# Performance work log

Hardware: AMD Instinct MI355X
Metric: run time of the kernel (lower is better)

The kernel has to match this reference:

```python
import jax, jax.numpy as jnp
import numpy as np

V, E, HID, T = 50000, 256, 512, 12   # vocab, embed dim, lstm hidden (bi total), tagset size
START, STOP = 10, 11
L = 2048                              # sentence length
H = HID // 2                          # per-direction hidden
NEG = -10000.0


def setup_inputs():
    key = jax.random.key(0)
    ks = jax.random.split(key, 13)
    s = 0.05
    sentence = jax.random.randint(ks[0], (L,), 0, V)
    embed = jax.random.normal(ks[1], (V, E), jnp.float32) * s
    w_ih_f = jax.random.normal(ks[2], (4 * H, E), jnp.float32) * s
    w_hh_f = jax.random.normal(ks[3], (4 * H, H), jnp.float32) * s
    b_ih_f = jax.random.normal(ks[4], (4 * H,), jnp.float32) * s
    b_hh_f = jax.random.normal(ks[5], (4 * H,), jnp.float32) * s
    w_ih_b = jax.random.normal(ks[6], (4 * H, E), jnp.float32) * s
    w_hh_b = jax.random.normal(ks[7], (4 * H, H), jnp.float32) * s
    b_ih_b = jax.random.normal(ks[8], (4 * H,), jnp.float32) * s
    b_hh_b = jax.random.normal(ks[9], (4 * H,), jnp.float32) * s
    w_out = jax.random.normal(ks[10], (T, HID), jnp.float32) * s
    b_out = jax.random.normal(ks[11], (T,), jnp.float32) * s
    transitions = jax.random.normal(ks[12], (T, T), jnp.float32)
    transitions = transitions.at[START, :].set(NEG).at[:, STOP].set(NEG)
    return dict(sentence=sentence, embed=embed,
                w_ih_f=w_ih_f, w_hh_f=w_hh_f, b_ih_f=b_ih_f, b_hh_f=b_hh_f,
                w_ih_b=w_ih_b, w_hh_b=w_hh_b, b_ih_b=b_ih_b, b_hh_b=b_hh_b,
                w_out=w_out, b_out=b_out, transitions=transitions)


def _lstm_dir(x, w_ih, w_hh, b, reverse):
    # x: [L, E] -> hs: [L, H]; PyTorch gate order i, f, g, o
    xg = x @ w_ih.T + b  # [L, 4H] precomputed input contribution

    def step(carry, xg_t):
        h, c = carry
        g = xg_t + h @ w_hh.T
        i, f, gg, o = jnp.split(g, 4)
        i, f, o = jax.nn.sigmoid(i), jax.nn.sigmoid(f), jax.nn.sigmoid(o)
        c = f * c + i * jnp.tanh(gg)
        h = o * jnp.tanh(c)
        return (h, c), h

    hdim = w_hh.shape[1]
    init = (jnp.zeros((hdim,), x.dtype), jnp.zeros((hdim,), x.dtype))
    _, hs = jax.lax.scan(step, init, xg, reverse=reverse)
    return hs


def _lstm_feats(sentence, embed, w_ih_f, w_hh_f, b_ih_f, b_hh_f,
                w_ih_b, w_hh_b, b_ih_b, b_hh_b, w_out, b_out):
    x = embed[sentence]                                        # [L, E]
    hf = _lstm_dir(x, w_ih_f, w_hh_f, b_ih_f + b_hh_f, False)  # [L, H]
    hb = _lstm_dir(x, w_ih_b, w_hh_b, b_ih_b + b_hh_b, True)   # [L, H]
    h = jnp.concatenate([hf, hb], axis=-1)                     # [L, 2H]
    return h @ w_out.T + b_out                                 # [L, T]


def reference(sentence, embed, w_ih_f, w_hh_f, b_ih_f, b_hh_f,
              w_ih_b, w_hh_b, b_ih_b, b_hh_b, w_out, b_out, transitions):
    feats = _lstm_feats(sentence, embed, w_ih_f, w_hh_f, b_ih_f, b_hh_f,
                        w_ih_b, w_hh_b, b_ih_b, b_hh_b, w_out, b_out)

    # Viterbi DP vectorized over tags, scanned over time
    init_v = jnp.full((T,), NEG, feats.dtype).at[START].set(0.0)

    def vstep(v, feat):
        scores = transitions + v[None, :]        # [next_tag, prev_tag]
        bp = jnp.argmax(scores, axis=1)          # best previous tag per next tag
        v_new = jnp.max(scores, axis=1) + feat
        return v_new, bp

    v, bps = jax.lax.scan(vstep, init_v, feats)  # bps: [L, T]
    terminal = v + transitions[STOP]
    best = jnp.argmax(terminal)
    path_score = terminal[best]

    def btrack(tag, bp):
        return bp[tag], tag

    _, best_path = jax.lax.scan(btrack, best, bps, reverse=True)  # [L] tags
    return path_score, best_path
```

## Files before the change

### kernel.cpp

```cpp
#include <hip/hip_runtime.h>

#define LSEQ 2048
#define TAGS 12

typedef _Float16 half2v __attribute__((ext_vector_type(2)));
typedef unsigned long long u64;

__device__ __forceinline__ float sigm(float x){ return 1.0f/(1.0f+__expf(-x)); }
__device__ __forceinline__ float tanh_fast(float x){ return 1.0f - 2.0f/(1.0f+__expf(2.0f*x)); }
__device__ __forceinline__ half2v pack2(float a, float b){
  half2v r; r.x=(_Float16)a; r.y=(_Float16)b; return r;
}

__global__ void init_kernel(u64* ex)
{
  int tid = blockIdx.x*256 + threadIdx.x;
  if (tid < 1024) ex[tid] = 0ull;
}

__global__ void xg_kernel(
    const int* sent, const float* embed,
    const float* w_ih_f, const float* b_ih_f, const float* b_hh_f,
    const float* w_ih_b, const float* b_ih_b, const float* b_hh_b,
    float* xg)
{
  __shared__ float x_sh[8][256];
  int tid = threadIdx.x;
  int t0 = blockIdx.x * 8;
  for (int i=0;i<8;++i){
    int idx = sent[t0+i];
    x_sh[i][tid] = embed[(size_t)idx*256 + tid];
  }
  __syncthreads();
  for (int ri=0; ri<8; ++ri){
    int r = ri*256 + tid;
    int d = r >> 10;
    int row = r & 1023;
    const float* wr = (d ? w_ih_b : w_ih_f) + (size_t)row*256;
    const float* bi = d ? b_ih_b : b_ih_f;
    const float* bh = d ? b_hh_b : b_hh_f;
    float acc[8];
    #pragma unroll
    for (int i=0;i<8;++i) acc[i]=0.f;
    for (int k0=0;k0<256;k0+=4){
      float4 p = *(const float4*)(wr + k0);
      #pragma unroll
      for (int i=0;i<8;++i){
        acc[i] += p.x*x_sh[i][k0] + p.y*x_sh[i][k0+1]
                + p.z*x_sh[i][k0+2] + p.w*x_sh[i][k0+3];
      }
    }
    float bias = bi[row] + bh[row];
    #pragma unroll
    for (int i=0;i<8;++i)
      xg[((size_t)d*LSEQ + (size_t)(t0+i))*1024 + row] = acc[i] + bias;
  }
}

__global__ __launch_bounds__(256,1) void lstm_rec(
    const float* __restrict__ w_hh_f, const float* __restrict__ w_hh_b,
    const float* __restrict__ xg, unsigned short* __restrict__ hstH,
    u64* __restrict__ ex)
{
  int blk = blockIdx.x;
  int d = blk & 7;
  if (d > 1) return;
  int q = blk >> 3;
  int qa = (q+1)&3, qb = (q+2)&3, qc = (q+3)&3;

  int tid = threadIdx.x;
  int g = tid >> 6, l = tid & 63;
  int row = g*256 + 64*q + l;
  const float* W = d ? w_hh_b : w_hh_f;
  const float* xgd = xg + (size_t)d*LSEQ*1024;
  unsigned short* hd = hstH + (size_t)d*LSEQ*256;
  u64* exd = ex + (size_t)d*256;

  __shared__ float gate_sh[256];
  __shared__ unsigned h2all[128];

  half2v w[128];
  {
    const float* p0 = W + (size_t)row*256 + 64*q;
    const float* p1 = W + (size_t)row*256 + 64*qa;
    const float* p2 = W + (size_t)row*256 + 64*qb;
    const float* p3 = W + (size_t)row*256 + 64*qc;
    #pragma unroll
    for (int k0=0;k0<16;++k0){
      float4 a = *(const float4*)(p0+4*k0);
      w[2*k0]      = pack2(a.x,a.y);  w[2*k0+1]    = pack2(a.z,a.w);
      float4 b = *(const float4*)(p1+4*k0);
      w[32+2*k0]   = pack2(b.x,b.y);  w[32+2*k0+1] = pack2(b.z,b.w);
      float4 cc= *(const float4*)(p2+4*k0);
      w[64+2*k0]   = pack2(cc.x,cc.y); w[64+2*k0+1] = pack2(cc.z,cc.w);
      float4 e = *(const float4*)(p3+4*k0);
      w[96+2*k0]   = pack2(e.x,e.y);  w[96+2*k0+1] = pack2(e.z,e.w);
    }
  }
  if (tid < 128) h2all[tid] = 0u;
  float c0 = 0.f, c1 = 0.f;
  unsigned hp = 0u;

  int pollj = tid - 64;
  int pollpeer = (q + 1 + (pollj>>5)) & 3;
  int pollslot = 32*pollpeer + (pollj & 31);
  int adrA = (l < 32) ? (32*qa + l) : (32*qb + (l-32));
  int adrB = 32*qc + (l & 31);
  int adrL = 32*q + (l & 31);
  __syncthreads();

  int tf = d ? (LSEQ-1) : 0;
  float xg0 = xgd[(size_t)tf*1024 + row];

  for (int s=0;s<LSEQ;++s){
    if (s > 0 && tid < 32){
      atomicExch(&exd[((s&1)<<7) + 32*q + tid], ((u64)(unsigned)s << 32) | (u64)hp);
      int tp = d ? (LSEQ-s) : (s-1);
      *(unsigned*)&hd[(size_t)tp*256 + 64*q + 2*tid] = hp;
    }
    u64 v0 = 0ull;
    bool poller = (s > 0) && (tid >= 64) && (tid < 160);
    if (poller)
      v0 = __hip_atomic_load(&exd[((s&1)<<7) + pollslot],
                             __ATOMIC_RELAXED, __HIP_MEMORY_SCOPE_AGENT);
    unsigned hl = h2all[adrL];
    float a0=xg0, a1=0.f, a2=0.f, a3=0.f;
    #pragma unroll
    for (int k=0;k<32;k+=4){
      unsigned p0v = __builtin_amdgcn_readlane(hl,k);
      unsigned p1v = __builtin_amdgcn_readlane(hl,k+1);
      unsigned p2v = __builtin_amdgcn_readlane(hl,k+2);
      unsigned p3v = __builtin_amdgcn_readlane(hl,k+3);
      a0 = __builtin_amdgcn_fdot2(__builtin_bit_cast(half2v,p0v), w[k],   a0, false);
      a1 = __builtin_amdgcn_fdot2(__builtin_bit_cast(half2v,p1v), w[k+1], a1, false);
      a2 = __builtin_amdgcn_fdot2(__builtin_bit_cast(half2v,p2v), w[k+2], a2, false);
      a3 = __builtin_amdgcn_fdot2(__builtin_bit_cast(half2v,p3v), w[k+3], a3, false);
    }
    if (poller){
      u64 v = v0;
      while ((unsigned)(v>>32) != (unsigned)s)
        v = __hip_atomic_load(&exd[((s&1)<<7) + pollslot],
                              __ATOMIC_RELAXED, __HIP_MEMORY_SCOPE_AGENT);
      h2all[pollslot] = (unsigned)v;
    }
    float nxg = 0.f;
    if (s+1 < LSEQ){
      int tn = d ? (LSEQ-2-s) : (s+1);
      nxg = xgd[(size_t)tn*1024 + row];
    }
    __syncthreads();
    unsigned hrA = h2all[adrA];
    unsigned hrB = h2all[adrB];
    #pragma unroll
    for (int k=0;k<32;k+=2){
      unsigned pA0 = __builtin_amdgcn_readlane(hrA, k);
      unsigned pA1 = __builtin_amdgcn_readlane(hrA, k+1);
      unsigned pB0 = __builtin_amdgcn_readlane(hrA, 32+k);
      unsigned pB1 = __builtin_amdgcn_readlane(hrA, 32+k+1);
      unsigned pC0 = __builtin_amdgcn_readlane(hrB, k);
      unsigned pC1 = __builtin_amdgcn_readlane(hrB, k+1);
      a0 = __builtin_amdgcn_fdot2(__builtin_bit_cast(half2v,pA0), w[32+k],   a0, false);
      a1 = __builtin_amdgcn_fdot2(__builtin_bit_cast(half2v,pA1), w[32+k+1], a1, false);
      a2 = __builtin_amdgcn_fdot2(__builtin_bit_cast(half2v,pB0), w[64+k],   a2, false);
      a3 = __builtin_amdgcn_fdot2(__builtin_bit_cast(half2v,pB1), w[64+k+1], a3, false);
      a0 = __builtin_amdgcn_fdot2(__builtin_bit_cast(half2v,pC0), w[96+k],   a0, false);
      a1 = __builtin_amdgcn_fdot2(__builtin_bit_cast(half2v,pC1), w[96+k+1], a1, false);
    }
    float pre = (a0+a1) + (a2+a3);
    float act = (g==2) ? tanh_fast(pre) : sigm(pre);
    gate_sh[tid] = act;
    xg0 = nxg;
    __syncthreads();
    if (tid < 32){
      int m = tid;
      float2 gi = *(const float2*)&gate_sh[      2*m];
      float2 gf = *(const float2*)&gate_sh[ 64 + 2*m];
      float2 gg = *(const float2*)&gate_sh[128 + 2*m];
      float2 go = *(const float2*)&gate_sh[192 + 2*m];
      c0 = gf.x*c0 + gi.x*gg.x;
      c1 = gf.y*c1 + gi.y*gg.y;
      float h0 = go.x * tanh_fast(c0);
      float h1 = go.y * tanh_fast(c1);
      hp = __builtin_bit_cast(unsigned, pack2(h0,h1));
      h2all[32*q + m] = hp;
    }
    __syncthreads();
  }
  if (tid < 32){
    int tl = d ? 0 : (LSEQ-1);
    *(unsigned*)&hd[(size_t)tl*256 + 64*q + 2*tid] = hp;
  }
}

__global__ void feats_kernel(
    const unsigned short* hstH, const float* w_out, const float* b_out,
    float* feats)
{
  __shared__ float w_sh[12*520];
  __shared__ float h_sh[16*520];
  const _Float16* hf = (const _Float16*)hstH;
  int tid=threadIdx.x;
  int t0=blockIdx.x*16;
  for (int i=tid;i<12*512;i+=256){ int tag=i>>9,k=i&511; w_sh[tag*520+k]=w_out[i]; }
  for (int i=tid;i<16*512;i+=256){
    int tt=i>>9,k=i&511;
    float v = (k<256)? (float)hf[(size_t)(t0+tt)*256+k]
                     : (float)hf[(size_t)(LSEQ+t0+tt)*256 + (k-256)];
    h_sh[tt*520+k]=v;
  }
  __syncthreads();
  if (tid<192){
    int tt=tid/12, tag=tid%12;
    const float* wr=&w_sh[tag*520];
    const float* hr=&h_sh[tt*520];
    float acc=b_out[tag];
    for (int k=0;k<512;k+=4){
      float4 a=*(const float4*)(wr+k);
      float4 b=*(const float4*)(hr+k);
      acc += a.x*b.x+a.y*b.y+a.z*b.z+a.w*b.w;
    }
    feats[(size_t)(t0+tt)*12+tag]=acc;
  }
}

__global__ void BiLSTM_CRF_14405320311361_kernel(
    const float* feats, const float* trans, float* outp)
{
  __shared__ float fsh[LSEQ*12];
  __shared__ unsigned char bps[LSEQ*12];
  __shared__ float term_sh[16];
  __shared__ int ibuf[66];
  __shared__ unsigned char fmap[64*12];
  int tid = threadIdx.x;
  for (int i=tid; i<LSEQ*12/4; i+=256)
    *(float4*)&fsh[4*i] = *(const float4*)&feats[4*i];
  __syncthreads();

  int lane = tid & 63;
  int fl = (lane<12) ? lane : 0;
  float vn = 0.f;
  if (tid < 64){
    float tr[12];
    #pragma unroll
    for (int p=0;p<12;++p) tr[p] = trans[fl*12+p];
    vn = (lane==10) ? 0.f : -10000.f;
    float fa = fsh[fl];
    float fb = fsh[12+fl];
    for (int t=0;t<LSEQ;++t){
      unsigned vu = __float_as_uint(vn);
      float best; int bp; float sc;
      best = tr[0] + __uint_as_float(__builtin_amdgcn_readlane(vu,0)); bp = 0;
      sc = tr[1]  + __uint_as_float(__builtin_amdgcn_readlane(vu,1));  if(sc>best){best=sc;bp=1;}
      sc = tr[2]  + __uint_as_float(__builtin_amdgcn_readlane(vu,2));  if(sc>best){best=sc;bp=2;}
      sc = tr[3]  + __uint_as_float(__builtin_amdgcn_readlane(vu,3));  if(sc>best){best=sc;bp=3;}
      sc = tr[4]  + __uint_as_float(__builtin_amdgcn_readlane(vu,4));  if(sc>best){best=sc;bp=4;}
      sc = tr[5]  + __uint_as_float(__builtin_amdgcn_readlane(vu,5));  if(sc>best){best=sc;bp=5;}
      sc = tr[6]  + __uint_as_float(__builtin_amdgcn_readlane(vu,6));  if(sc>best){best=sc;bp=6;}
      sc = tr[7]  + __uint_as_float(__builtin_amdgcn_readlane(vu,7));  if(sc>best){best=sc;bp=7;}
      sc = tr[8]  + __uint_as_float(__builtin_amdgcn_readlane(vu,8));  if(sc>best){best=sc;bp=8;}
      sc = tr[9]  + __uint_as_float(__builtin_amdgcn_readlane(vu,9));  if(sc>best){best=sc;bp=9;}
      sc = tr[10] + __uint_as_float(__builtin_amdgcn_readlane(vu,10)); if(sc>best){best=sc;bp=10;}
      sc = tr[11] + __uint_as_float(__builtin_amdgcn_readlane(vu,11)); if(sc>best){best=sc;bp=11;}
      vn = best + fa;
      fa = fb;
      if (t+2 < LSEQ) fb = fsh[(t+2)*12+fl];
      if (lane<12) bps[t*12+lane] = (unsigned char)bp;
    }
  }
  if (tid < 12) term_sh[tid] = vn + trans[11*12+tid];
  __syncthreads();
  if (tid == 0){
    float bs=term_sh[0]; int bt=0;
    for (int p=1;p<12;++p){ if (term_sh[p]>bs){bs=term_sh[p];bt=p;} }
    outp[0] = bs;
    ibuf[64] = bt;
  }
  __syncthreads();
  if (tid < 64){
    int b = tid;
    int f[12];
    int thi = b*32+31;
    #pragma unroll
    for (int x=0;x<12;++x) f[x] = bps[thi*12+x];
    for (int t=thi-1; t>=b*32; --t){
      int base = t*12;
      #pragma unroll
      for (int x=0;x<12;++x) f[x] = bps[base + f[x]];
    }
    #pragma unroll
    for (int x=0;x<12;++x) fmap[b*12+x] = (unsigned char)f[x];
  }
  __syncthreads();
  if (tid == 0){
    int tag = ibuf[64];
    for (int b=63;b>=0;--b){ ibuf[b]=tag; tag = fmap[b*12+tag]; }
  }
  __syncthreads();
  if (tid < 64){
    int b = tid;
    int tag = ibuf[b];
    for (int t=b*32+31; t>=b*32; --t){
      outp[1+t] = (float)tag;
      tag = bps[t*12+tag];
    }
  }
}

extern "C" void kernel_launch(void* const* d_in, const int* in_sizes, int n_in,
                              void* d_out, int out_size, void* d_ws, size_t ws_size,
                              hipStream_t stream) {
  const int*   sent   = (const int*)d_in[0];
  const float* embed  = (const float*)d_in[1];
  const float* w_ih_f = (const float*)d_in[2];
  const float* w_hh_f = (const float*)d_in[3];
  const float* b_ih_f = (const float*)d_in[4];
  const float* b_hh_f = (const float*)d_in[5];
  const float* w_ih_b = (const float*)d_in[6];
  const float* w_hh_b = (const float*)d_in[7];
  const float* b_ih_b = (const float*)d_in[8];
  const float* b_hh_b = (const float*)d_in[9];
  const float* w_out  = (const float*)d_in[10];
  const float* b_out  = (const float*)d_in[11];
  const float* trans  = (const float*)d_in[12];

  float* xg = (float*)d_ws;
  unsigned short* hstH = (unsigned short*)(xg + (size_t)2*LSEQ*1024);
  u64* ex = (u64*)(hstH + (size_t)2*LSEQ*256);
  float* feats = (float*)(ex + 1024);
  float* outp  = (float*)d_out;

  init_kernel<<<dim3(4), dim3(256), 0, stream>>>(ex);
  xg_kernel<<<dim3(LSEQ/8), dim3(256), 0, stream>>>(
      sent, embed, w_ih_f, b_ih_f, b_hh_f, w_ih_b, b_ih_b, b_hh_b, xg);
  lstm_rec<<<dim3(32), dim3(256), 0, stream>>>(w_hh_f, w_hh_b, xg, hstH, ex);
  feats_kernel<<<dim3(LSEQ/16), dim3(256), 0, stream>>>(hstH, w_out, b_out, feats);
  BiLSTM_CRF_14405320311361_kernel<<<dim3(1), dim3(256), 0, stream>>>(feats, trans, outp);
}
```

Baseline: 3.540 ms.

## Drop per-step barrier, compute cell state redundantly, and read remote h via vector LDS

Every wavefront now recomputes the cell update for its 32 lanes, so each wave holds its own local h in a register. This removes the final per-step __syncthreads and the shared h write. Remote h values are kept in a compact shared buffer and read with 16-byte vector loads instead of readlane broadcasts. The publish to peers moves to the end of the step as a relaxed atomic store rather than an atomicExch at the start of the next step. The init kernel is folded into the xg kernel to save a launch. Relying on the two remaining barriers to order the h2rem and gate_sh reuse across steps is subtle and could race.

New measurement: 3.551 ms. No clear change (+0.3%).

```diff
diff --git a/kernel.cpp b/kernel.cpp
--- a/kernel.cpp
+++ b/kernel.cpp
@@ -12,20 +12,18 @@
   half2v r; r.x=(_Float16)a; r.y=(_Float16)b; return r;
 }
 
-__global__ void init_kernel(u64* ex)
-{
-  int tid = blockIdx.x*256 + threadIdx.x;
-  if (tid < 1024) ex[tid] = 0ull;
-}
-
 __global__ void xg_kernel(
     const int* sent, const float* embed,
     const float* w_ih_f, const float* b_ih_f, const float* b_hh_f,
     const float* w_ih_b, const float* b_ih_b, const float* b_hh_b,
-    float* xg)
+    float* xg, u64* ex)
 {
   __shared__ float x_sh[8][256];
   int tid = threadIdx.x;
+  if (blockIdx.x == 0){
+    #pragma unroll
+    for (int i=0;i<4;++i) ex[tid + 256*i] = 0ull;
+  }
   int t0 = blockIdx.x * 8;
   for (int i=0;i<8;++i){
     int idx = sent[t0+i];
@@ -70,6 +68,7 @@
 
   int tid = threadIdx.x;
   int g = tid >> 6, l = tid & 63;
+  int m = l & 31;
   int row = g*256 + 64*q + l;
   const float* W = d ? w_hh_b : w_hh_f;
   const float* xgd = xg + (size_t)d*LSEQ*1024;
@@ -77,7 +76,7 @@
   u64* exd = ex + (size_t)d*256;
 
   __shared__ float gate_sh[256];
-  __shared__ unsigned h2all[128];
+  __shared__ __align__(16) unsigned h2rem[96];
 
   half2v w[128];
   {
@@ -97,33 +96,25 @@
       w[96+2*k0]   = pack2(e.x,e.y);  w[96+2*k0+1] = pack2(e.z,e.w);
     }
   }
-  if (tid < 128) h2all[tid] = 0u;
+  if (tid < 96) h2rem[tid] = 0u;
   float c0 = 0.f, c1 = 0.f;
-  unsigned hp = 0u;
+  unsigned hl = 0u;
 
   int pollj = tid - 64;
   int pollpeer = (q + 1 + (pollj>>5)) & 3;
   int pollslot = 32*pollpeer + (pollj & 31);
-  int adrA = (l < 32) ? (32*qa + l) : (32*qb + (l-32));
-  int adrB = 32*qc + (l & 31);
-  int adrL = 32*q + (l & 31);
+  bool isPoller = (tid >= 64) && (tid < 160);
   __syncthreads();
 
   int tf = d ? (LSEQ-1) : 0;
   float xg0 = xgd[(size_t)tf*1024 + row];
 
   for (int s=0;s<LSEQ;++s){
-    if (s > 0 && tid < 32){
-      atomicExch(&exd[((s&1)<<7) + 32*q + tid], ((u64)(unsigned)s << 32) | (u64)hp);
-      int tp = d ? (LSEQ-s) : (s-1);
-      *(unsigned*)&hd[(size_t)tp*256 + 64*q + 2*tid] = hp;
-    }
     u64 v0 = 0ull;
-    bool poller = (s > 0) && (tid >= 64) && (tid < 160);
-    if (poller)
+    bool poll = (s > 0) && isPoller;
+    if (poll)
       v0 = __hip_atomic_load(&exd[((s&1)<<7) + pollslot],
                              __ATOMIC_RELAXED, __HIP_MEMORY_SCOPE_AGENT);
-    unsigned hl = h2all[adrL];
     float a0=xg0, a1=0.f, a2=0.f, a3=0.f;
     #pragma unroll
     for (int k=0;k<32;k+=4){
@@ -136,12 +127,12 @@
       a2 = __builtin_amdgcn_fdot2(__builtin_bit_cast(half2v,p2v), w[k+2], a2, false);
       a3 = __builtin_amdgcn_fdot2(__builtin_bit_cast(half2v,p3v), w[k+3], a3, false);
     }
-    if (poller){
+    if (poll){
       u64 v = v0;
       while ((unsigned)(v>>32) != (unsigned)s)
         v = __hip_atomic_load(&exd[((s&1)<<7) + pollslot],
                               __ATOMIC_RELAXED, __HIP_MEMORY_SCOPE_AGENT);
-      h2all[pollslot] = (unsigned)v;
+      h2rem[pollj] = (unsigned)v;
     }
     float nxg = 0.f;
     if (s+1 < LSEQ){
@@ -149,30 +140,20 @@
       nxg = xgd[(size_t)tn*1024 + row];
     }
     __syncthreads();
-    unsigned hrA = h2all[adrA];
-    unsigned hrB = h2all[adrB];
-    #pragma unroll
-    for (int k=0;k<32;k+=2){
-      unsigned pA0 = __builtin_amdgcn_readlane(hrA, k);
-      unsigned pA1 = __builtin_amdgcn_readlane(hrA, k+1);
-      unsigned pB0 = __builtin_amdgcn_readlane(hrA, 32+k);
-      unsigned pB1 = __builtin_amdgcn_readlane(hrA, 32+k+1);
-      unsigned pC0 = __builtin_amdgcn_readlane(hrB, k);
-      unsigned pC1 = __builtin_amdgcn_readlane(hrB, k+1);
-      a0 = __builtin_amdgcn_fdot2(__builtin_bit_cast(half2v,pA0), w[32+k],   a0, false);
-      a1 = __builtin_amdgcn_fdot2(__builtin_bit_cast(half2v,pA1), w[32+k+1], a1, false);
-      a2 = __builtin_amdgcn_fdot2(__builtin_bit_cast(half2v,pB0), w[64+k],   a2, false);
-      a3 = __builtin_amdgcn_fdot2(__builtin_bit_cast(half2v,pB1), w[64+k+1], a3, false);
-      a0 = __builtin_amdgcn_fdot2(__builtin_bit_cast(half2v,pC0), w[96+k],   a0, false);
-      a1 = __builtin_amdgcn_fdot2(__builtin_bit_cast(half2v,pC1), w[96+k+1], a1, false);
+    #pragma unroll
+    for (int j=0;j<24;++j){
+      uint4 hv = *(const uint4*)&h2rem[4*j];
+      a0 = __builtin_amdgcn_fdot2(__builtin_bit_cast(half2v,hv.x), w[32+4*j],   a0, false);
+      a1 = __builtin_amdgcn_fdot2(__builtin_bit_cast(half2v,hv.y), w[32+4*j+1], a1, false);
+      a2 = __builtin_amdgcn_fdot2(__builtin_bit_cast(half2v,hv.z), w[32+4*j+2], a2, false);
+      a3 = __builtin_amdgcn_fdot2(__builtin_bit_cast(half2v,hv.w), w[32+4*j+3], a3, false);
     }
     float pre = (a0+a1) + (a2+a3);
     float act = (g==2) ? tanh_fast(pre) : sigm(pre);
     gate_sh[tid] = act;
     xg0 = nxg;
     __syncthreads();
-    if (tid < 32){
-      int m = tid;
+    {
       float2 gi = *(const float2*)&gate_sh[      2*m];
       float2 gf = *(const float2*)&gate_sh[ 64 + 2*m];
       float2 gg = *(const float2*)&gate_sh[128 + 2*m];
@@ -181,14 +162,16 @@
       c1 = gf.y*c1 + gi.y*gg.y;
       float h0 = go.x * tanh_fast(c0);
       float h1 = go.y * tanh_fast(c1);
-      hp = __builtin_bit_cast(unsigned, pack2(h0,h1));
-      h2all[32*q + m] = hp;
-    }
-    __syncthreads();
-  }
-  if (tid < 32){
-    int tl = d ? 0 : (LSEQ-1);
-    *(unsigned*)&hd[(size_t)tl*256 + 64*q + 2*tid] = hp;
+      hl = __builtin_bit_cast(unsigned, pack2(h0,h1));
+    }
+    if (tid < 32){
+      if (s+1 < LSEQ)
+        __hip_atomic_store(&exd[(((s+1)&1)<<7) + 32*q + tid],
+                           ((u64)(unsigned)(s+1) << 32) | (u64)hl,
+                           __ATOMIC_RELAXED, __HIP_MEMORY_SCOPE_AGENT);
+      int tp = d ? (LSEQ-1-s) : s;
+      *(unsigned*)&hd[(size_t)tp*256 + 64*q + 2*tid] = hl;
+    }
   }
 }
 
@@ -329,9 +312,8 @@
   float* feats = (float*)(ex + 1024);
   float* outp  = (float*)d_out;
 
-  init_kernel<<<dim3(4), dim3(256), 0, stream>>>(ex);
   xg_kernel<<<dim3(LSEQ/8), dim3(256), 0, stream>>>(
-      sent, embed, w_ih_f, b_ih_f, b_hh_f, w_ih_b, b_ih_b, b_hh_b, xg);
+      sent, embed, w_ih_f, b_ih_f, b_hh_f, w_ih_b, b_ih_b, b_hh_b, xg, ex);
   lstm_rec<<<dim3(32), dim3(256), 0, stream>>>(w_hh_f, w_hh_b, xg, hstH, ex);
   feats_kernel<<<dim3(LSEQ/16), dim3(256), 0, stream>>>(hstH, w_out, b_out, feats);
   BiLSTM_CRF_14405320311361_kernel<<<dim3(1), dim3(256), 0, stream>>>(feats, trans, outp);
```
